# Kernel optimization log

Hardware: AMD Instinct MI355X
Metric: run time of the kernel (lower is better)

The kernel has to match this reference:

```python
import jax, jax.numpy as jnp
import numpy as np

N_NODES = 80000; N_EDGES = 480000; F_IN = 5; DIM = 3; HID = 128; LAT = 128
N_POOLS = 2; RATIO = 0.5; SLOPE = 0.2  # GATv2 leaky_relu negative slope


def _p(key, shape, fan_in):
    return jax.random.normal(key, shape, dtype=jnp.float32) / np.sqrt(float(fan_in))


def setup_inputs() -> dict:
    key = jax.random.key(0)
    ks = jax.random.split(key, 20)
    c0 = F_IN + DIM + 3          # conv0 in-channels: x | pos | y*ones
    ch = HID + DIM               # all later convs / pool gnns: h | pos
    return dict(
        x=jax.random.normal(ks[0], (N_NODES, F_IN), dtype=jnp.float32),
        y=jax.random.normal(ks[1], (1,), dtype=jnp.float32),
        pos=jax.random.normal(ks[2], (N_NODES, DIM), dtype=jnp.float32),
        edge_index=jax.random.randint(ks[3], (2, N_EDGES), 0, N_NODES),
        Wl0=_p(ks[4], (c0, HID), c0), Wr0=_p(ks[5], (c0, HID), c0),
        We0=_p(ks[6], (DIM, HID), DIM), a0=_p(ks[7], (HID,), HID), b0=jnp.zeros((HID,), jnp.float32),
        # stacked convs: [conv1, pool-conv1, pool-conv2, last-conv], all (HID+DIM)->HID(=LAT)
        Wls=_p(ks[8], (4, ch, HID), ch), Wrs=_p(ks[9], (4, ch, HID), ch),
        Wes=_p(ks[10], (4, DIM, HID), DIM), atts=_p(ks[11], (4, HID), HID), bs=jnp.zeros((4, HID), jnp.float32),
        # SAGPool score GNNs: (HID+DIM)->1
        pWl=_p(ks[12], (N_POOLS, ch, 1), ch), pWr=_p(ks[13], (N_POOLS, ch, 1), ch),
        pWe=_p(ks[14], (N_POOLS, DIM, 1), DIM), pa=_p(ks[15], (N_POOLS, 1), 1), pb=jnp.zeros((N_POOLS, 1), jnp.float32),
        linW=_p(ks[16], (LAT, LAT), LAT), linb=jnp.zeros((LAT,), jnp.float32),
    )


def _gatv2(xf, ei, ea, Wl, Wr, We, att, b):
    # PyG GATv2Conv, heads=1, add_self_loops=True, fill_value='mean' for loop edge_attr
    N = xf.shape[0]
    src = jnp.asarray(ei[0]); dst = jnp.asarray(ei[1])
    ones = jnp.ones((src.shape[0],), dtype=xf.dtype)
    deg = jax.ops.segment_sum(ones, dst, num_segments=N)
    loop_attr = jax.ops.segment_sum(ea, dst, num_segments=N) / jnp.clip(deg, 1.0)[:, None]
    ar = jnp.arange(N)
    src_f = jnp.concatenate([src, ar]); dst_f = jnp.concatenate([dst, ar])
    ea_f = jnp.concatenate([ea, loop_attr], axis=0)
    xl = xf @ Wl; xr = xf @ Wr                              # [N, C]
    m = jax.nn.leaky_relu(xl[src_f] + xr[dst_f] + ea_f @ We, SLOPE)  # [Ef, C]
    logits = m @ att                                        # [Ef]
    mx = jax.ops.segment_max(logits, dst_f, num_segments=N)
    z = jnp.exp(logits - mx[dst_f])
    denom = jax.ops.segment_sum(z, dst_f, num_segments=N)
    alpha = z / denom[dst_f]
    return jax.ops.segment_sum(alpha[:, None] * xl[src_f], dst_f, num_segments=N) + b


def _augment(ei, N):
    # adj + adj@adj (sparse coo with coalesce): union of 1-hop and 2-hop edges
    s, t = ei[0].astype(np.int64), ei[1].astype(np.int64)
    order = np.argsort(s, kind='stable')
    t2 = t[order]
    counts = np.bincount(s, minlength=N)
    starts = np.concatenate([[0], np.cumsum(counts)[:-1]])
    lens = counts[t]                      # out-degree of each edge's target (middle node)
    total = int(lens.sum())
    within = np.arange(total) - np.repeat(np.cumsum(lens) - lens, lens)
    b = t2[np.repeat(starts[t], lens) + within]
    a = np.repeat(s, lens)
    key = np.unique(np.concatenate([s * N + t, a * N + b]))
    return np.stack([key // N, key % N])


def _filter_adj(ei, perm, N):
    mask = np.zeros(N, dtype=bool); mask[perm] = True
    keep = mask[ei[0]] & mask[ei[1]]
    relabel = np.full(N, -1, dtype=np.int64); relabel[perm] = np.arange(len(perm))
    return relabel[ei[:, keep]]


def _encoder(fl, ei0, structs):
    (x, y, pos, Wl0, Wr0, We0, a0, b0, Wls, Wrs, Wes, atts, bs,
     pWl, pWr, pWe, pa, pb, linW, linb) = fl
    capture = structs is None
    recs = []
    ei = ei0
    ea = pos[ei[1]] - pos[ei[0]]
    h = jax.nn.elu(_gatv2(jnp.concatenate([x, pos, y * jnp.ones_like(pos)], 1), ei, ea, Wl0, Wr0, We0, a0, b0))
    h = jax.nn.elu(_gatv2(jnp.concatenate([h, pos], 1), ei, ea, Wls[0], Wrs[0], Wes[0], atts[0], bs[0]))
    pe = [ei]; pp = [pos]; eas = [ea]
    N = x.shape[0]
    for l in range(N_POOLS):
        ei_aug = _augment(np.asarray(ei), N) if capture else structs[l][0]
        ea_aug = pos[ei_aug[1]] - pos[ei_aug[0]]
        score = jnp.tanh(_gatv2(jnp.concatenate([h, pos], 1), ei_aug, ea_aug,
                                pWl[l], pWr[l], pWe[l], pa[l], pb[l])[:, 0])
        k = int(np.ceil(RATIO * N))
        if capture:
            _, perm = jax.lax.top_k(score, k)
            perm = np.asarray(perm)
            ei_next = _filter_adj(np.asarray(ei), perm, N)
            recs.append((ei_aug, perm, ei_next))
        else:
            _, perm, ei_next = structs[l]
        h = h[perm] * score[perm][:, None]
        pos = pos[perm]
        ei = ei_next; N = k
        ea = pos[ei[1]] - pos[ei[0]]
        pe.insert(0, ei); pp.insert(0, pos); eas.insert(0, ea)
        h = jax.nn.elu(_gatv2(jnp.concatenate([h, pos], 1), ei, ea,
                              Wls[l + 1], Wrs[l + 1], Wes[l + 1], atts[l + 1], bs[l + 1]))
    h = jax.nn.elu(_gatv2(jnp.concatenate([h, pos], 1), ei, ea, Wls[3], Wrs[3], Wes[3], atts[3], bs[3]))
    out = h @ linW + linb   # torch.vmap(self.lin)
    return out, pe, pp, eas, recs


def reference(x, y, pos, edge_index, Wl0, Wr0, We0, a0, b0, Wls, Wrs, Wes, atts, bs,
              pWl, pWr, pWe, pa, pb, linW, linb):
    fl = (x, y, pos, Wl0, Wr0, We0, a0, b0, Wls, Wrs, Wes, atts, bs,
          pWl, pWr, pWe, pa, pb, linW, linb)
    out, pe, pp, eas, _ = _encoder(fl, np.asarray(edge_index), None)
    return (out,) + tuple(jnp.asarray(e) for e in pe) + tuple(pp) + tuple(eas)
```

## Files before the change

### kernel.cpp

```cpp
#include <hip/hip_runtime.h>

typedef unsigned long long ull;

#define NN0 80000
#define EE0 480000
#define KK1 40000
#define KK2 20000
#define FLATMAX 8000000
#define SCH 4096
#define CDIV(a,b) (((a)+(b)-1)/(b))
#define HBINS (1<<21)
#define LSW 1024
#define FCAP 512

#define C_E1 2
#define C_E2 3
#define C_M0 5
#define C_M1 6

__device__ __forceinline__ int getE(const int* p, int s){ if(!p) return s; int e=*p; return e<s? e : s; }
__device__ __forceinline__ float leakyf(float x){ return x>0.f? x : 0.2f*x; }
__device__ __forceinline__ double leakyd(double x){ return x>0.0? x : 0.2*x; }
__device__ __forceinline__ float eluf(float x){ return x>0.f? x : (expf(x)-1.f); }

__device__ __forceinline__ ull encd(double f){ ull u=(ull)__double_as_longlong(f); return (u>>63)? ~u : (u|0x8000000000000000ULL); }

template<int MODE, bool DUAL>
__global__ void gemm_k(const float* __restrict__ F1, const float* __restrict__ pos,
                       const float* __restrict__ yv,
                       const float* __restrict__ W1, const float* __restrict__ W2,
                       const float* __restrict__ bias,
                       float* __restrict__ O1, float* __restrict__ O2, int N)
{
  const int K = MODE==0? 11 : (MODE==1? 131 : 128);
  __shared__ float lf[32][132];
  int t = threadIdx.x;
  int row0 = blockIdx.x*32;

  if(MODE==0){
    for(int i=t;i<32*11;i+=256){
      int r=i/11, k=i-r*11; int row=row0+r;
      float f=0.f;
      if(row<N) f = (k<5)? F1[(size_t)row*5+k] : (k<8? pos[(size_t)row*3+(k-5)] : yv[0]);
      lf[r][k]=f;
    }
  } else {
    for(int i=t;i<32*32;i+=256){
      int r=i>>5, c4=i&31; int row=row0+r;
      float4 v; v.x=0.f;v.y=0.f;v.z=0.f;v.w=0.f;
      if(row<N) v = *(const float4*)(F1+(size_t)row*128+c4*4);
      *(float4*)(&lf[r][c4*4]) = v;
    }
    if(MODE==1){
      for(int i=t;i<32*3;i+=256){
        int r=i/3, d=i-r*3; int row=row0+r;
        lf[r][128+d] = (row<N)? pos[(size_t)row*3+d] : 0.f;
      }
    }
  }
  __syncthreads();

  int cg = t&31, rg = t>>5;
  int g = cg*4;
  int rbase = rg*4;

  float acc1[4][4]; float acc2[4][4];
  #pragma unroll
  for(int rr=0;rr<4;rr++)
    #pragma unroll
    for(int c=0;c<4;c++){ acc1[rr][c]=0.f; acc2[rr][c]=0.f; }

  #pragma unroll 4
  for(int k=0;k<K;k++){
    float4 w = *(const float4*)(W1 + (size_t)k*128 + g);
    float4 v; v.x=0.f;v.y=0.f;v.z=0.f;v.w=0.f;
    if(DUAL) v = *(const float4*)(W2 + (size_t)k*128 + g);
    #pragma unroll
    for(int rr=0;rr<4;rr++){
      float f = lf[rbase+rr][k];
      acc1[rr][0]+=f*w.x; acc1[rr][1]+=f*w.y; acc1[rr][2]+=f*w.z; acc1[rr][3]+=f*w.w;
      if(DUAL){ acc2[rr][0]+=f*v.x; acc2[rr][1]+=f*v.y; acc2[rr][2]+=f*v.z; acc2[rr][3]+=f*v.w; }
    }
  }

  float4 bb; bb.x=0.f;bb.y=0.f;bb.z=0.f;bb.w=0.f;
  if(bias) bb = *(const float4*)(bias+g);
  #pragma unroll
  for(int rr=0;rr<4;rr++){
    int row = row0 + rbase + rr;
    if(row<N){
      float4 r1; r1.x=acc1[rr][0]+bb.x; r1.y=acc1[rr][1]+bb.y; r1.z=acc1[rr][2]+bb.z; r1.w=acc1[rr][3]+bb.w;
      *(float4*)(O1+(size_t)row*128+g) = r1;
      if(DUAL){
        float4 r2; r2.x=acc2[rr][0]; r2.y=acc2[rr][1]; r2.z=acc2[rr][2]; r2.w=acc2[rr][3];
        *(float4*)(O2+(size_t)row*128+g) = r2;
      }
    }
  }
}

__global__ void scan_p1(const int* __restrict__ in, const int* pN, int Ns, int* __restrict__ bsums){
  __shared__ int red[256];
  int n = getE(pN,Ns);
  int base = blockIdx.x*SCH;
  int s=0;
  for(int i=base+threadIdx.x; i<base+SCH; i+=256) if(i<n) s+=in[i];
  red[threadIdx.x]=s; __syncthreads();
  for(int o=128;o;o>>=1){ if(threadIdx.x<(unsigned)o) red[threadIdx.x]+=red[threadIdx.x+o]; __syncthreads(); }
  if(threadIdx.x==0) bsums[blockIdx.x]=red[0];
}
__global__ void scan_p2(int* bsums, int nb){
  __shared__ int lds[256];
  int t=threadIdx.x;
  int v = (t<nb)? bsums[t] : 0;
  lds[t]=v; __syncthreads();
  for(int o=1;o<256;o<<=1){ int u=0; if(t>=o) u=lds[t-o]; __syncthreads(); lds[t]+=u; __syncthreads(); }
  if(t<nb) bsums[t]=lds[t]-v;
}
__global__ void scan_p3(const int* __restrict__ in, int* __restrict__ out, const int* pN, int Ns,
                        const int* __restrict__ bsums, int* total){
  __shared__ int tsum[256];
  int n = getE(pN,Ns);
  int base = blockIdx.x*SCH + threadIdx.x*16;
  int v[16]; int s=0;
  #pragma unroll
  for(int q=0;q<16;q++){ int i=base+q; int xv=(i<n)? in[i]:0; v[q]=s; s+=xv; }
  tsum[threadIdx.x]=s; __syncthreads();
  int mine=s;
  for(int o=1;o<256;o<<=1){ int u=0; if(threadIdx.x>=(unsigned)o) u=tsum[threadIdx.x-o]; __syncthreads(); tsum[threadIdx.x]+=u; __syncthreads(); }
  int pre = bsums[blockIdx.x] + tsum[threadIdx.x] - mine;
  #pragma unroll
  for(int q=0;q<16;q++){
    int i=base+q;
    if(i<=n){
      int val = pre+v[q];
      out[i]=val;
      if(i==n && total) *total=val;
    }
  }
}

__global__ void count_src(const int* __restrict__ es, const int* pE, int Es, int* cnts){
  int e = blockIdx.x*256+threadIdx.x; int E = getE(pE,Es); if(e>=E) return;
  atomicAdd(&cnts[es[e]], 1);
}
__global__ void fill_eord(const int* __restrict__ es, const int* __restrict__ ed, const int* pE, int Es,
                          const int* __restrict__ dstarts, int* cursor, int* insrc){
  int e = blockIdx.x*256+threadIdx.x; int E = getE(pE,Es); if(e>=E) return;
  int d = ed[e];
  int p = dstarts[d] + atomicAdd(&cursor[d],1);
  insrc[p] = es[e];
}

__global__ void feat_fused(const int* __restrict__ insrc, const int* __restrict__ dstarts,
                           const float* __restrict__ A, const float* __restrict__ B,
                           const float* __restrict__ pos,
                           const float* __restrict__ We, const float* __restrict__ att,
                           const float* __restrict__ bias, float* __restrict__ h, int N)
{
  __shared__ float lgAll[4][FCAP];
  int wv = threadIdx.x>>6, lane = threadIdx.x&63;
  int w = blockIdx.x*4 + wv;
  bool active = (w<N);
  if(!active) w = N-1;
  float* lg = lgAll[wv];
  int r0=dstarts[w], r1=dstarts[w+1]; int din=r1-r0;
  int c=lane, c2=lane+64;
  float B0 = B[(size_t)w*128+c], B1 = B[(size_t)w*128+c2];
  float We0c=We[c], We1c=We[128+c], We2c=We[256+c];
  float We0d=We[c2], We1d=We[128+c2], We2d=We[256+c2];
  float attc=att[c], attd=att[c2];
  float pw0=pos[w*3], pw1=pos[w*3+1], pw2=pos[w*3+2];

  float l0=0,l1=0,l2=0;
  for(int j=0;j<din;j++){
    int s = insrc[r0+j];
    float e0=pw0-pos[s*3], e1=pw1-pos[s*3+1], e2=pw2-pos[s*3+2];
    l0+=e0; l1+=e1; l2+=e2;
    float a0=A[(size_t)s*128+c], a1=A[(size_t)s*128+c2];
    float m1 = a0 + B0 + e0*We0c + e1*We1c + e2*We2c;
    float m2 = a1 + B1 + e0*We0d + e1*We1d + e2*We2d;
    float p = leakyf(m1)*attc + leakyf(m2)*attd;
    for(int o=32;o;o>>=1) p += __shfl_down(p,o,64);
    if(lane==0 && j<FCAP) lg[j]=p;
  }
  float inv = 1.f/fmaxf((float)din, 1.f);
  float q0=l0*inv, q1=l1*inv, q2=l2*inv;
  float a0w=A[(size_t)w*128+c], a1w=A[(size_t)w*128+c2];
  float pself;
  {
    float m1 = a0w + B0 + q0*We0c + q1*We1c + q2*We2c;
    float m2 = a1w + B1 + q0*We0d + q1*We1d + q2*We2d;
    float p = leakyf(m1)*attc + leakyf(m2)*attd;
    for(int o=32;o;o>>=1) p += __shfl_down(p,o,64);
    pself = __shfl(p,0,64);
  }
  float mx = pself;
  int dc = din<FCAP? din : FCAP;
  for(int j=lane;j<dc;j+=64) mx = fmaxf(mx, lg[j]);
  for(int o=32;o;o>>=1) mx = fmaxf(mx, __shfl_down(mx,o,64));
  mx = __shfl(mx,0,64);
  for(int j=FCAP;j<din;j++){
    int s = insrc[r0+j];
    float e0=pw0-pos[s*3], e1=pw1-pos[s*3+1], e2=pw2-pos[s*3+2];
    float a0=A[(size_t)s*128+c], a1=A[(size_t)s*128+c2];
    float m1 = a0 + B0 + e0*We0c + e1*We1c + e2*We2c;
    float m2 = a1 + B1 + e0*We0d + e1*We1d + e2*We2d;
    float p = leakyf(m1)*attc + leakyf(m2)*attd;
    for(int o=32;o;o>>=1) p += __shfl_down(p,o,64);
    p = __shfl(p,0,64);
    mx = fmaxf(mx, p);
  }

  float denom=0.f, acc0=0.f, acc1=0.f;
  for(int j=0;j<din;j++){
    int s = insrc[r0+j];
    float lgj;
    if(j<FCAP) lgj = lg[j];
    else {
      float e0=pw0-pos[s*3], e1=pw1-pos[s*3+1], e2=pw2-pos[s*3+2];
      float a0=A[(size_t)s*128+c], a1=A[(size_t)s*128+c2];
      float m1 = a0 + B0 + e0*We0c + e1*We1c + e2*We2c;
      float m2 = a1 + B1 + e0*We0d + e1*We1d + e2*We2d;
      float p = leakyf(m1)*attc + leakyf(m2)*attd;
      for(int o=32;o;o>>=1) p += __shfl_down(p,o,64);
      lgj = __shfl(p,0,64);
    }
    float z = expf(lgj - mx);
    denom += z;
    acc0 += z*A[(size_t)s*128+c];
    acc1 += z*A[(size_t)s*128+c2];
  }
  {
    float z = expf(pself - mx);
    denom += z;
    acc0 += z*a0w; acc1 += z*a1w;
  }
  float iv = 1.f/denom;
  float b0v=bias[c], b1v=bias[c2];
  acc0 = eluf(acc0*iv + b0v); acc1 = eluf(acc1*iv + b1v);
  if(active){
    h[(size_t)w*128+c ] = acc0;
    h[(size_t)w*128+c2] = acc1;
  }
}

__global__ void gemm_score(const float* __restrict__ h, const float* __restrict__ pos,
                           const float* __restrict__ pWl, const float* __restrict__ pWr,
                           double* __restrict__ xls, double* __restrict__ xrs, int N)
{
  int t = threadIdx.x;
  int lane = t&31;
  int n = blockIdx.x*8 + (t>>5);
  if(n>=N) return;
  double sl=0, sr=0;
  #pragma unroll
  for(int q=0;q<4;q++){
    int k = lane + q*32;
    double f = (double)h[(size_t)n*128+k];
    sl += f*(double)pWl[k]; sr += f*(double)pWr[k];
  }
  if(lane<3){
    double f = (double)pos[n*3+lane];
    sl += f*(double)pWl[128+lane]; sr += f*(double)pWr[128+lane];
  }
  for(int o=16;o;o>>=1){ sl += __shfl_down(sl,o,32); sr += __shfl_down(sr,o,32); }
  if(lane==0){ xls[n]=sl; xrs[n]=sr; }
}

__global__ void score_fused2(const int* __restrict__ insrc, const int* __restrict__ dstarts,
                             const float* __restrict__ pos,
                             const double* __restrict__ xls, const double* __restrict__ xrs,
                             const float* __restrict__ pWe, const float* __restrict__ paP,
                             const float* __restrict__ pbP,
                             double* __restrict__ score, int N)
{
  __shared__ int lsAll[4][LSW];
  int wv = threadIdx.x>>6;
  int lane = threadIdx.x&63;
  int w = blockIdx.x*4 + wv;
  bool active = (w<N);
  if(!active) w = N-1;
  int* ls = lsAll[wv];
  int r0=dstarts[w], r1=dstarts[w+1]; int din=r1-r0;
  for(int j=lane;j<din && j<LSW;j+=64) ls[j]=insrc[r0+j];
  __syncthreads();
  int off = din<LSW? din : LSW;
  for(int base=0; base<din && base<LSW; base+=64){
    int t = base + lane;
    int u0=0, len=0;
    if(t<din && t<LSW){
      int u = ls[t];
      u0 = dstarts[u]; len = dstarts[u+1]-u0;
    }
    int pre = len;
    #pragma unroll
    for(int o=1;o<64;o<<=1){ int v=__shfl_up(pre,o,64); if(lane>=o) pre+=v; }
    int tot = __shfl(pre, 63, 64);
    int myoff = off + pre - len;
    for(int j=0;j<len;j++){ int p=myoff+j; if(p<LSW) ls[p]=insrc[u0+j]; }
    off += tot;
  }
  int d = off<LSW? off : LSW;
  __syncthreads();

  float pd0=pos[w*3], pd1=pos[w*3+1], pd2=pos[w*3+2];
  double w0=(double)pWe[0], w1=(double)pWe[1], w2=(double)pWe[2], pa=(double)paP[0];
  double xrd=xrs[w];
  ull umask=0;
  double lgv[4], xv[4];
  double mx=-1e300, s0=0,s1=0,s2=0; int ucnt=0;
  #pragma unroll
  for(int it=0; it<4; it++){
    int j = lane + it*64;
    if(j<d){
      int s = ls[j];
      bool uniq = true;
      for(int q=0;q<j;q++) if(ls[q]==s){ uniq=false; break; }
      if(uniq){
        umask |= 1ULL<<it;
        ucnt++;
        double e0=(double)(pd0-pos[s*3]), e1=(double)(pd1-pos[s*3+1]), e2=(double)(pd2-pos[s*3+2]);
        s0+=e0; s1+=e1; s2+=e2;
        double xl = xls[s];
        double lg = leakyd(xl+xrd + e0*w0+e1*w1+e2*w2) * pa;
        lgv[it]=lg; xv[it]=xl;
        mx = fmax(mx, lg);
      }
    }
  }
  int nb=4;
  for(int j=lane+256; j<d; j+=64, nb++){
    int s = ls[j];
    bool uniq = true;
    for(int q=0;q<j;q++) if(ls[q]==s){ uniq=false; break; }
    if(uniq){
      umask |= 1ULL<<nb;
      ucnt++;
      double e0=(double)(pd0-pos[s*3]), e1=(double)(pd1-pos[s*3+1]), e2=(double)(pd2-pos[s*3+2]);
      s0+=e0; s1+=e1; s2+=e2;
      double lg = leakyd(xls[s]+xrd + e0*w0+e1*w1+e2*w2) * pa;
      mx = fmax(mx, lg);
    }
  }
  for(int o=32;o;o>>=1){
    mx = fmax(mx, __shfl_down(mx,o,64));
    s0 += __shfl_down(s0,o,64);
    s1 += __shfl_down(s1,o,64);
    s2 += __shfl_down(s2,o,64);
    ucnt += __shfl_down(ucnt,o,64);
  }
  mx=__shfl(mx,0,64); s0=__shfl(s0,0,64); s1=__shfl(s1,0,64); s2=__shfl(s2,0,64); ucnt=__shfl(ucnt,0,64);
  double invd = 1.0/(double)(ucnt>0? ucnt : 1);
  double lg_self = leakyd(xls[w]+xrd + (s0*invd)*w0 + (s1*invd)*w1 + (s2*invd)*w2) * pa;
  mx = fmax(mx, lg_self);
  double den=0, acc=0;
  #pragma unroll
  for(int it=0; it<4; it++){
    if((umask>>it)&1ULL){
      double z = exp(lgv[it]-mx);
      den += z; acc += z*xv[it];
    }
  }
  nb=4;
  for(int j=lane+256; j<d; j+=64, nb++){
    if((umask>>nb)&1ULL){
      int s = ls[j];
      double e0=(double)(pd0-pos[s*3]), e1=(double)(pd1-pos[s*3+1]), e2=(double)(pd2-pos[s*3+2]);
      double lg = leakyd(xls[s]+xrd + e0*w0+e1*w1+e2*w2) * pa;
      double z = exp(lg-mx);
      den += z; acc += z*xls[s];
    }
  }
  for(int o=32;o;o>>=1){
    den += __shfl_down(den,o,64);
    acc += __shfl_down(acc,o,64);
  }
  if(lane==0 && active){
    double z = exp(lg_self-mx);
    den += z; acc += z*xls[w];
    score[w] = tanh(acc/den + (double)pbP[0]);
  }
}

__global__ void enc_scores(const double* __restrict__ score, int N, ull* __restrict__ ek,
                           int* __restrict__ rank){
  int i = blockIdx.x*256+threadIdx.x; if(i>=N) return;
  ek[i] = encd(score[i]);
  rank[i] = 0x3f3f3f3f;
}
__global__ void hist_g(const ull* __restrict__ ek, int N, int shift, const ull* __restrict__ selT,
                       int* __restrict__ hist){
  int i = blockIdx.x*256+threadIdx.x; if(i>=N) return;
  ull key = ek[i];
  if(shift+21 < 64){
    if((key >> (shift+21)) != ((*selT) >> (shift+21))) return;
  }
  atomicAdd(&hist[(int)((key>>shift)&0x1FFFFF)], 1);
}
__global__ void part21(const int* __restrict__ hist, int* __restrict__ partial){
  __shared__ int red[256];
  int b = blockIdx.x;
  int s=0;
  for(int i=threadIdx.x;i<1024;i+=256) s += hist[b*1024+i];
  red[threadIdx.x]=s; __syncthreads();
  for(int o=128;o;o>>=1){ if(threadIdx.x<(unsigned)o) red[threadIdx.x]+=red[threadIdx.x+o]; __syncthreads(); }
  if(threadIdx.x==0) partial[b]=red[0];
}
__global__ void findbin_g(const int* __restrict__ partial, const int* __restrict__ hist,
                          ull* __restrict__ selT, int* __restrict__ selRB, int k, int shift){
  __shared__ int ts[256];
  __shared__ int cstar, rbase;
  int t=threadIdx.x;
  int keff = k - *selRB;
  int s8[8]; int mysum=0;
  #pragma unroll
  for(int q=0;q<8;q++){ s8[q]=partial[t*8+q]; mysum+=s8[q]; }
  ts[t]=mysum; __syncthreads();
  for(int o=1;o<256;o<<=1){ int u=(t+o<256)? ts[t+o]:0; __syncthreads(); ts[t]+=u; __syncthreads(); }
  int after = (t<255)? ts[t+1] : 0;
  if(ts[t] >= keff && after < keff){
    int run = after;
    for(int q=7;q>=0;q--){
      if(run < keff && run + s8[q] >= keff){ cstar = t*8+q; rbase = run; }
      run += s8[q];
    }
  }
  __syncthreads();
  int cs=cstar, rb=rbase;
  int b4[4]; int ms=0;
  #pragma unroll
  for(int q=0;q<4;q++){ b4[q]=hist[cs*1024 + t*4 + q]; ms+=b4[q]; }
  ts[t]=ms; __syncthreads();
  for(int o=1;o<256;o<<=1){ int u=(t+o<256)? ts[t+o]:0; __syncthreads(); ts[t]+=u; __syncthreads(); }
  int after2 = (t<255)? ts[t+1] : 0;
  if(rb+ts[t] >= keff && rb+after2 < keff){
    int run = rb+after2;
    for(int q=3;q>=0;q--){
      if(run < keff && run + b4[q] >= keff){
        *selT |= ((ull)(cs*1024 + t*4 + q)) << shift;
        *selRB = (k - keff) + run;
      }
      run += b4[q];
    }
  }
}
__global__ void rank_hist(const ull* __restrict__ ek, int N, const ull* __restrict__ selT,
                          int* __restrict__ hist){
  int i = blockIdx.x*256+threadIdx.x; if(i>=N) return;
  ull key = ek[i]; if(key < *selT) return;
  int dg = (int)((~key >> 43) & 0x1FFFFF);
  atomicAdd(&hist[dg], 1);
}
__global__ void binscan(const int* __restrict__ hist, const int* __restrict__ p2,
                        int* __restrict__ binstarts){
  __shared__ int ts[256];
  int b = blockIdx.x, t = threadIdx.x;
  int v[4]; int s=0;
  #pragma unroll
  for(int q=0;q<4;q++){ v[q]=s; s+=hist[b*1024 + t*4 + q]; }
  ts[t]=s; __syncthreads();
  int mine=s;
  for(int o=1;o<256;o<<=1){ int u=0; if(t>=(unsigned)o) u=ts[t-o]; __syncthreads(); ts[t]+=u; __syncthreads(); }
  int pre = p2[b] + ts[t] - mine;
  #pragma unroll
  for(int q=0;q<4;q++) binstarts[b*1024 + t*4 + q] = pre + v[q];
  if(b==2047 && t==255) binstarts[HBINS] = p2[b] + ts[255];
}
__global__ void rank_fill(const ull* __restrict__ ek, int N, const ull* __restrict__ selT,
                          const int* __restrict__ binstarts, int* __restrict__ hist,
                          ull* __restrict__ mkeys, int* __restrict__ midx){
  int i = blockIdx.x*256+threadIdx.x; if(i>=N) return;
  ull key = ek[i]; if(key < *selT) return;
  int dg = (int)((~key >> 43) & 0x1FFFFF);
  int o = atomicSub(&hist[dg], 1) - 1;
  int p = binstarts[dg] + o;
  mkeys[p] = key; midx[p] = i;
}
__global__ void rank_within(const int* __restrict__ binstarts,
                            const ull* __restrict__ mkeys, const int* __restrict__ midx,
                            int* __restrict__ rank, int Nmax){
  int m = blockIdx.x*256+threadIdx.x; if(m>=Nmax) return;
  int total = binstarts[HBINS]; if(m>=total) return;
  ull key = mkeys[m]; int ii = midx[m];
  int dg = (int)((~key >> 43) & 0x1FFFFF);
  int s = binstarts[dg], e = binstarts[dg+1];
  int cnt = 0;
  for(int j=s;j<e;j++){
    ull kj = mkeys[j];
    cnt += (kj > key) || (kj == key && midx[j] < ii);
  }
  rank[ii] = s + cnt;
}
__global__ void scatter_perm(const int* __restrict__ rank, int N, int k, int* __restrict__ perm){
  int i = blockIdx.x*256+threadIdx.x; if(i>=N) return;
  int r = rank[i]; if(r<k) perm[r]=i;
}
__global__ void pool_gather(const float* __restrict__ h, const double* __restrict__ score,
                            const int* __restrict__ perm, int k, float* __restrict__ outA){
  int idx = blockIdx.x*256+threadIdx.x; if(idx>=k*32) return;
  int r = idx>>5, g = (idx&31)*4;
  int p = perm[r]; float sc = (float)score[p];
  const float4 x = *(const float4*)(h + (size_t)p*128 + g);
  float4 o; o.x=x.x*sc; o.y=x.y*sc; o.z=x.z*sc; o.w=x.w*sc;
  *(float4*)(outA + (size_t)r*128 + g) = o;
}
__global__ void pos_gather(const float* __restrict__ posc, const int* __restrict__ perm, int k, float* __restrict__ posn){
  int idx = blockIdx.x*256+threadIdx.x; if(idx>=k*3) return;
  int r = idx/3, j = idx-r*3;
  posn[idx] = posc[perm[r]*3+j];
}

__global__ void filter_flags(const int* __restrict__ es, const int* __restrict__ ed, const int* pE, int Es,
                             const int* __restrict__ rank, int k, int* __restrict__ flags){
  int e = blockIdx.x*256+threadIdx.x; int E = getE(pE,Es); if(e>=E) return;
  flags[e] = (rank[es[e]]<k && rank[ed[e]]<k) ? 1 : 0;
}
__global__ void filter_write(const int* __restrict__ es, const int* __restrict__ ed, const int* pE, int Es,
                             const int* __restrict__ rank, int k, const int* __restrict__ scanout,
                             int* __restrict__ ns, int* __restrict__ nd){
  int e = blockIdx.x*256+threadIdx.x; int E = getE(pE,Es); if(e>=E) return;
  int rs = rank[es[e]], rd = rank[ed[e]];
  if(rs<k && rd<k){ int p = scanout[e]; ns[p]=rs; nd[p]=rd; }
}

__global__ void calc_offsets(const int* __restrict__ cnt, long long* __restrict__ offs){
  if(blockIdx.x==0 && threadIdx.x==0){
    long long E1 = cnt[C_E1], E2 = cnt[C_E2];
    long long o = (long long)KK2*128;
    offs[0]=0;
    offs[1]=o; o += 2*E2;
    offs[2]=o; o += 2*E1;
    offs[3]=o; o += 2*(long long)EE0;
    offs[4]=o; o += (long long)KK2*3;
    offs[5]=o; o += (long long)KK1*3;
    offs[6]=o; o += (long long)NN0*3;
    offs[7]=o; o += 3*E2;
    offs[8]=o; o += 3*E1;
    offs[9]=o;
  }
}
__global__ void emit_pe(const int* __restrict__ s, const int* __restrict__ d, const int* pE, int Es,
                        const long long* __restrict__ offs, int oi, float* __restrict__ out){
  int e = blockIdx.x*256+threadIdx.x; int E = getE(pE,Es); if(e>=E) return;
  long long o = offs[oi];
  out[o+e]   = (float)s[e];
  out[o+E+e] = (float)d[e];
}
__global__ void emit_pp(const float* __restrict__ p, int n, const long long* __restrict__ offs, int oi, float* __restrict__ out){
  int i = blockIdx.x*256+threadIdx.x; if(i>=n) return;
  out[offs[oi]+i] = p[i];
}
__global__ void emit_eas(const int* __restrict__ s, const int* __restrict__ d, const int* pE, int Es,
                         const float* __restrict__ pos, const long long* __restrict__ offs, int oi, float* __restrict__ out){
  int e = blockIdx.x*256+threadIdx.x; int E = getE(pE,Es); if(e>=E) return;
  long long o = offs[oi];
  int ss=s[e], dd=d[e];
  out[o+3*e+0] = pos[dd*3+0]-pos[ss*3+0];
  out[o+3*e+1] = pos[dd*3+1]-pos[ss*3+1];
  out[o+3*e+2] = pos[dd*3+2]-pos[ss*3+2];
}

extern "C" void kernel_launch(void* const* d_in, const int* in_sizes, int n_in,
                              void* d_out, int out_size, void* d_ws, size_t ws_size,
                              hipStream_t stream)
{
  const float* x    = (const float*)d_in[0];
  const float* yv   = (const float*)d_in[1];
  const float* pos0 = (const float*)d_in[2];
  const int*   ei   = (const int*)d_in[3];
  const float* Wl0  = (const float*)d_in[4];
  const float* Wr0  = (const float*)d_in[5];
  const float* We0  = (const float*)d_in[6];
  const float* a0   = (const float*)d_in[7];
  const float* b0   = (const float*)d_in[8];
  const float* Wls  = (const float*)d_in[9];
  const float* Wrs  = (const float*)d_in[10];
  const float* Wes  = (const float*)d_in[11];
  const float* atts = (const float*)d_in[12];
  const float* bs   = (const float*)d_in[13];
  const float* pWl  = (const float*)d_in[14];
  const float* pWr  = (const float*)d_in[15];
  const float* pWe  = (const float*)d_in[16];
  const float* pa   = (const float*)d_in[17];
  const float* pb   = (const float*)d_in[18];
  const float* linW = (const float*)d_in[19];
  const float* linb = (const float*)d_in[20];
  float* out = (float*)d_out;

  const int* eisrc = ei;
  const int* eidst = ei + EE0;

  char* base = (char*)d_ws; size_t off = 0;
  auto alloc = [&](size_t b)->void*{
    off = (off + 255) & ~(size_t)255;
    void* p = base + off; off += b; return p;
  };
  int*       cnt     = (int*)alloc(64*4);
  long long* offs    = (long long*)alloc(16*8);
  int*       bsums   = (int*)alloc(256*4);
  ull*       sel     = (ull*)alloc(2*8);
  int*       hist    = (int*)alloc((size_t)HBINS*4);
  int*       partial = (int*)alloc(2048*4);
  int*       partial2= (int*)alloc(2304*4);
  double*    xls     = (double*)alloc((size_t)NN0*8);
  double*    xrs     = (double*)alloc((size_t)NN0*8);
  double*    score   = (double*)alloc((size_t)NN0*8);
  ull*       ek      = (ull*)alloc((size_t)NN0*8);
  int*       rank    = (int*)alloc((size_t)NN0*4);
  int*       perm    = (int*)alloc((size_t)NN0*4);
  int*       cursor  = (int*)alloc((size_t)NN0*4);
  int*       ccnt    = (int*)alloc((size_t)NN0*4);
  int*       dstarts = (int*)alloc((size_t)(NN0+1)*4);
  int*       insrc   = (int*)alloc((size_t)EE0*4);
  int*       flags   = (int*)alloc((size_t)EE0*4);
  int*       scanout = (int*)alloc((size_t)(EE0+1)*4);
  int*       eb0s    = (int*)alloc((size_t)EE0*4);
  int*       eb0d    = (int*)alloc((size_t)EE0*4);
  int*       eb1s    = (int*)alloc((size_t)EE0*4);
  int*       eb1d    = (int*)alloc((size_t)EE0*4);
  float*     pos1    = (float*)alloc((size_t)KK1*12);
  float*     pos2    = (float*)alloc((size_t)KK2*12);
  float*     A       = (float*)alloc((size_t)NN0*128*4);
  float*     B       = (float*)alloc((size_t)NN0*128*4);
  float*     h       = (float*)alloc((size_t)NN0*128*4);
  void*      uni     = alloc((size_t)(EE0+FLATMAX)*8);
  if(off > ws_size) return;

  int*    binstarts= (int*)uni;
  ull*    mkeys    = (ull*)((int*)uni + (HBINS + 256));
  int*    midx     = (int*)(mkeys + NN0);
  ull*    selT  = sel;
  int*    selRB = (int*)(sel+1);

  hipMemsetAsync(cnt, 0, 64*4, stream);

  auto scan = [&](const int* in, int* sout, const int* pN, int Ns, int* total){
    int nb = CDIV(Ns+1, SCH);
    scan_p1<<<nb,256,0,stream>>>(in,pN,Ns,bsums);
    scan_p2<<<1,256,0,stream>>>(bsums,nb);
    scan_p3<<<nb,256,0,stream>>>(in,sout,pN,Ns,bsums,total);
  };

  auto build_csr_dst = [&](const int* es, const int* ed, const int* pE, int Emax, int N){
    hipMemsetAsync(ccnt,0,(size_t)N*4,stream);
    count_src<<<CDIV(Emax,256),256,0,stream>>>(ed,pE,Emax,ccnt);
    scan(ccnt,dstarts,nullptr,N,nullptr);
    hipMemsetAsync(cursor,0,(size_t)N*4,stream);
    fill_eord<<<CDIV(Emax,256),256,0,stream>>>(es,ed,pE,Emax,dstarts,cursor,insrc);
  };

  auto feat_conv = [&](const float* Wl, const float* Wr, const float* We, const float* att, const float* bias,
                       int N, const float* pcur, bool conv0mode){
    if(conv0mode)
      gemm_k<0,true><<<CDIV(N,32),256,0,stream>>>(x,pcur,yv,Wl,Wr,nullptr,A,B,N);
    else
      gemm_k<1,true><<<CDIV(N,32),256,0,stream>>>(h,pcur,nullptr,Wl,Wr,nullptr,A,B,N);
    feat_fused<<<CDIV(N,4),256,0,stream>>>(insrc,dstarts,A,B,pcur,We,att,bias,h,N);
  };

  auto pool = [&](int l, int N, int k, const int* es, const int* ed, const int* pE, int Emax,
                  const float* pcur, float* pnext, int* ns, int* nd, int eslot){
    gemm_score<<<CDIV(N,8),256,0,stream>>>(h,pcur,pWl+l*131,pWr+l*131,xls,xrs,N);
    score_fused2<<<CDIV(N,4),256,0,stream>>>(insrc,dstarts,pcur,xls,xrs,pWe+l*3,pa+l,pb+l,score,N);
    enc_scores<<<CDIV(N,256),256,0,stream>>>(score,N,ek,rank);
    hipMemsetAsync(sel,0,16,stream);
    for(int r=0;r<2;r++){
      int sh = 43 - 21*r;
      hipMemsetAsync(hist,0,(size_t)HBINS*4,stream);
      hist_g<<<CDIV(N,256),256,0,stream>>>(ek,N,sh,selT,hist);
      part21<<<2048,256,0,stream>>>(hist,partial);
      findbin_g<<<1,256,0,stream>>>(partial,hist,selT,selRB,k,sh);
    }
    hipMemsetAsync(hist,0,(size_t)HBINS*4,stream);
    rank_hist  <<<CDIV(N,256),256,0,stream>>>(ek,N,selT,hist);
    part21     <<<2048,256,0,stream>>>(hist,partial);
    scan(partial,partial2,nullptr,2048,nullptr);
    binscan    <<<2048,256,0,stream>>>(hist,partial2,binstarts);
    rank_fill  <<<CDIV(N,256),256,0,stream>>>(ek,N,selT,binstarts,hist,mkeys,midx);
    rank_within<<<CDIV(N,256),256,0,stream>>>(binstarts,mkeys,midx,rank,N);
    scatter_perm<<<CDIV(N,256),256,0,stream>>>(rank,N,k,perm);
    pool_gather<<<CDIV(k*32,256),256,0,stream>>>(h,score,perm,k,A);
    hipMemcpyAsync(h,A,(size_t)k*128*4,hipMemcpyDeviceToDevice,stream);
    pos_gather<<<CDIV(k*3,256),256,0,stream>>>(pcur,perm,k,pnext);
    filter_flags<<<CDIV(Emax,256),256,0,stream>>>(es,ed,pE,Emax,rank,k,flags);
    scan(flags,scanout,pE,Emax,cnt+eslot);
    filter_write<<<CDIV(Emax,256),256,0,stream>>>(es,ed,pE,Emax,rank,k,scanout,ns,nd);
  };

  build_csr_dst(eisrc,eidst,nullptr,EE0, NN0);
  feat_conv(Wl0,Wr0,We0,a0,b0, NN0, pos0, true);
  feat_conv(Wls+0*16768,Wrs+0*16768,Wes+0*384,atts+0*128,bs+0*128, NN0, pos0, false);
  pool(0, NN0, KK1, eisrc,eidst,nullptr,EE0, pos0,pos1, eb0s,eb0d, C_E1);
  build_csr_dst(eb0s,eb0d,cnt+C_E1,EE0, KK1);
  feat_conv(Wls+1*16768,Wrs+1*16768,Wes+1*384,atts+1*128,bs+1*128, KK1, pos1, false);
  pool(1, KK1, KK2, eb0s,eb0d,cnt+C_E1,EE0, pos1,pos2, eb1s,eb1d, C_E2);
  build_csr_dst(eb1s,eb1d,cnt+C_E2,EE0, KK2);
  feat_conv(Wls+2*16768,Wrs+2*16768,Wes+2*384,atts+2*128,bs+2*128, KK2, pos2, false);
  feat_conv(Wls+3*16768,Wrs+3*16768,Wes+3*384,atts+3*128,bs+3*128, KK2, pos2, false);
  gemm_k<2,false><<<CDIV(KK2,32),256,0,stream>>>(h,nullptr,nullptr,linW,nullptr,linb,out,nullptr,KK2);

  calc_offsets<<<1,32,0,stream>>>(cnt,offs);
  emit_pe <<<CDIV(EE0,256),256,0,stream>>>(eb1s,eb1d,cnt+C_E2,EE0,offs,1,out);
  emit_pe <<<CDIV(EE0,256),256,0,stream>>>(eb0s,eb0d,cnt+C_E1,EE0,offs,2,out);
  emit_pe <<<CDIV(EE0,256),256,0,stream>>>(eisrc,eidst,nullptr,EE0,offs,3,out);
  emit_pp <<<CDIV(KK2*3,256),256,0,stream>>>(pos2,KK2*3,offs,4,out);
  emit_pp <<<CDIV(KK1*3,256),256,0,stream>>>(pos1,KK1*3,offs,5,out);
  emit_pp <<<CDIV(NN0*3,256),256,0,stream>>>(pos0,NN0*3,offs,6,out);
  emit_eas<<<CDIV(EE0,256),256,0,stream>>>(eb1s,eb1d,cnt+C_E2,EE0,pos2,offs,7,out);
  emit_eas<<<CDIV(EE0,256),256,0,stream>>>(eb0s,eb0d,cnt+C_E1,EE0,pos1,offs,8,out);
  emit_eas<<<CDIV(EE0,256),256,0,stream>>>(eisrc,eidst,nullptr,EE0,pos0,offs,9,out);
}
```

Measured before the change: 1.805 ms.

## Fuse edge-filter with scan, fold score encoding, batch output emit kernels

Replaces the flag/scan/write edge-filter pipeline with a two-pass fused scan that recomputes the rank predicate and writes compacted edges directly, removing the flags and scanout buffers. Score encoding moves into the score kernel, and rank initialisation becomes a memset. The first histogram clear is hoisted out of the pool loop. The nine output emit launches are merged into three launches using a y-grid dimension. This cuts kernel launches and global traffic in exchange for recomputing the rank lookups in two passes, and it relies on the histogram being zero again when the second pool starts.

```diff
diff --git a/kernel.cpp b/kernel.cpp
--- a/kernel.cpp
+++ b/kernel.cpp
@@ -137,6 +137,50 @@
       out[i]=val;
       if(i==n && total) *total=val;
     }
+  }
+}
+
+__global__ void fscan_p1(const int* __restrict__ es, const int* __restrict__ ed, const int* pE, int Es,
+                         const int* __restrict__ rank, int k, int* __restrict__ bsums){
+  __shared__ int red[256];
+  int n = getE(pE,Es);
+  int base = blockIdx.x*SCH;
+  int s=0;
+  for(int i=base+threadIdx.x; i<base+SCH; i+=256)
+    if(i<n) s += (rank[es[i]]<k && rank[ed[i]]<k) ? 1 : 0;
+  red[threadIdx.x]=s; __syncthreads();
+  for(int o=128;o;o>>=1){ if(threadIdx.x<(unsigned)o) red[threadIdx.x]+=red[threadIdx.x+o]; __syncthreads(); }
+  if(threadIdx.x==0) bsums[blockIdx.x]=red[0];
+}
+__global__ void fscan_p3(const int* __restrict__ es, const int* __restrict__ ed, const int* pE, int Es,
+                         const int* __restrict__ rank, int k, const int* __restrict__ bsums,
+                         int* __restrict__ ns, int* __restrict__ nd, int* total){
+  __shared__ int tsum[256];
+  int n = getE(pE,Es);
+  int base = blockIdx.x*SCH + threadIdx.x*16;
+  int v[16]; int rs[16], rd[16]; unsigned fm=0; int s=0;
+  #pragma unroll
+  for(int q=0;q<16;q++){
+    int i=base+q; int xv=0;
+    if(i<n){
+      int a=rank[es[i]], b=rank[ed[i]];
+      rs[q]=a; rd[q]=b;
+      if(a<k && b<k){ xv=1; fm |= 1u<<q; }
+    }
+    v[q]=s; s+=xv;
+  }
+  tsum[threadIdx.x]=s; __syncthreads();
+  int mine=s;
+  for(int o=1;o<256;o<<=1){ int u=0; if(threadIdx.x>=(unsigned)o) u=tsum[threadIdx.x-o]; __syncthreads(); tsum[threadIdx.x]+=u; __syncthreads(); }
+  int pre = bsums[blockIdx.x] + tsum[threadIdx.x] - mine;
+  #pragma unroll
+  for(int q=0;q<16;q++){
+    int i=base+q;
+    if(i<n && ((fm>>q)&1u)){
+      int p = pre+v[q];
+      ns[p]=rs[q]; nd[p]=rd[q];
+    }
+    if(i==n && total) *total = pre+v[q];
   }
 }
 
@@ -273,7 +317,7 @@
                              const double* __restrict__ xls, const double* __restrict__ xrs,
                              const float* __restrict__ pWe, const float* __restrict__ paP,
                              const float* __restrict__ pbP,
-                             double* __restrict__ score, int N)
+                             double* __restrict__ score, ull* __restrict__ ek, int N)
 {
   __shared__ int lsAll[4][LSW];
   int wv = threadIdx.x>>6;
@@ -379,16 +423,12 @@
   if(lane==0 && active){
     double z = exp(lg_self-mx);
     den += z; acc += z*xls[w];
-    score[w] = tanh(acc/den + (double)pbP[0]);
-  }
-}
-
-__global__ void enc_scores(const double* __restrict__ score, int N, ull* __restrict__ ek,
-                           int* __restrict__ rank){
-  int i = blockIdx.x*256+threadIdx.x; if(i>=N) return;
-  ek[i] = encd(score[i]);
-  rank[i] = 0x3f3f3f3f;
-}
+    double sc = tanh(acc/den + (double)pbP[0]);
+    score[w] = sc;
+    ek[w] = encd(sc);
+  }
+}
+
 __global__ void hist_g(const ull* __restrict__ ek, int N, int shift, const ull* __restrict__ selT,
                        int* __restrict__ hist){
   int i = blockIdx.x*256+threadIdx.x; if(i>=N) return;
@@ -509,19 +549,6 @@
   int idx = blockIdx.x*256+threadIdx.x; if(idx>=k*3) return;
   int r = idx/3, j = idx-r*3;
   posn[idx] = posc[perm[r]*3+j];
-}
-
-__global__ void filter_flags(const int* __restrict__ es, const int* __restrict__ ed, const int* pE, int Es,
-                             const int* __restrict__ rank, int k, int* __restrict__ flags){
-  int e = blockIdx.x*256+threadIdx.x; int E = getE(pE,Es); if(e>=E) return;
-  flags[e] = (rank[es[e]]<k && rank[ed[e]]<k) ? 1 : 0;
-}
-__global__ void filter_write(const int* __restrict__ es, const int* __restrict__ ed, const int* pE, int Es,
-                             const int* __restrict__ rank, int k, const int* __restrict__ scanout,
-                             int* __restrict__ ns, int* __restrict__ nd){
-  int e = blockIdx.x*256+threadIdx.x; int E = getE(pE,Es); if(e>=E) return;
-  int rs = rank[es[e]], rd = rank[ed[e]];
-  if(rs<k && rd<k){ int p = scanout[e]; ns[p]=rs; nd[p]=rd; }
 }
 
 __global__ void calc_offsets(const int* __restrict__ cnt, long long* __restrict__ offs){
@@ -540,20 +567,44 @@
     offs[9]=o;
   }
 }
-__global__ void emit_pe(const int* __restrict__ s, const int* __restrict__ d, const int* pE, int Es,
-                        const long long* __restrict__ offs, int oi, float* __restrict__ out){
-  int e = blockIdx.x*256+threadIdx.x; int E = getE(pE,Es); if(e>=E) return;
+__global__ void emit3_pe(const int* __restrict__ s2, const int* __restrict__ d2, const int* pE2,
+                         const int* __restrict__ s1, const int* __restrict__ d1, const int* pE1,
+                         const int* __restrict__ s0, const int* __restrict__ d0,
+                         const long long* __restrict__ offs, float* __restrict__ out){
+  int e = blockIdx.x*256+threadIdx.x;
+  int L = blockIdx.y;
+  const int* s; const int* d; int E; int oi;
+  if(L==0){ s=s2; d=d2; E=getE(pE2,EE0); oi=1; }
+  else if(L==1){ s=s1; d=d1; E=getE(pE1,EE0); oi=2; }
+  else { s=s0; d=d0; E=EE0; oi=3; }
+  if(e>=E) return;
   long long o = offs[oi];
   out[o+e]   = (float)s[e];
   out[o+E+e] = (float)d[e];
 }
-__global__ void emit_pp(const float* __restrict__ p, int n, const long long* __restrict__ offs, int oi, float* __restrict__ out){
-  int i = blockIdx.x*256+threadIdx.x; if(i>=n) return;
+__global__ void emit3_pp(const float* __restrict__ p2, const float* __restrict__ p1,
+                         const float* __restrict__ p0,
+                         const long long* __restrict__ offs, float* __restrict__ out){
+  int i = blockIdx.x*256+threadIdx.x;
+  int L = blockIdx.y;
+  const float* p; int n; int oi;
+  if(L==0){ p=p2; n=KK2*3; oi=4; }
+  else if(L==1){ p=p1; n=KK1*3; oi=5; }
+  else { p=p0; n=NN0*3; oi=6; }
+  if(i>=n) return;
   out[offs[oi]+i] = p[i];
 }
-__global__ void emit_eas(const int* __restrict__ s, const int* __restrict__ d, const int* pE, int Es,
-                         const float* __restrict__ pos, const long long* __restrict__ offs, int oi, float* __restrict__ out){
-  int e = blockIdx.x*256+threadIdx.x; int E = getE(pE,Es); if(e>=E) return;
+__global__ void emit3_eas(const int* __restrict__ s2, const int* __restrict__ d2, const int* pE2, const float* __restrict__ q2,
+                          const int* __restrict__ s1, const int* __restrict__ d1, const int* pE1, const float* __restrict__ q1,
+                          const int* __restrict__ s0, const int* __restrict__ d0, const float* __restrict__ q0,
+                          const long long* __restrict__ offs, float* __restrict__ out){
+  int e = blockIdx.x*256+threadIdx.x;
+  int L = blockIdx.y;
+  const int* s; const int* d; const float* pos; int E; int oi;
+  if(L==0){ s=s2; d=d2; pos=q2; E=getE(pE2,EE0); oi=7; }
+  else if(L==1){ s=s1; d=d1; pos=q1; E=getE(pE1,EE0); oi=8; }
+  else { s=s0; d=d0; pos=q0; E=EE0; oi=9; }
+  if(e>=E) return;
   long long o = offs[oi];
   int ss=s[e], dd=d[e];
   out[o+3*e+0] = pos[dd*3+0]-pos[ss*3+0];
@@ -613,8 +664,6 @@
   int*       ccnt    = (int*)alloc((size_t)NN0*4);
   int*       dstarts = (int*)alloc((size_t)(NN0+1)*4);
   int*       insrc   = (int*)alloc((size_t)EE0*4);
-  int*       flags   = (int*)alloc((size_t)EE0*4);
-  int*       scanout = (int*)alloc((size_t)(EE0+1)*4);
   int*       eb0s    = (int*)alloc((size_t)EE0*4);
   int*       eb0d    = (int*)alloc((size_t)EE0*4);
   int*       eb1s    = (int*)alloc((size_t)EE0*4);
@@ -634,6 +683,7 @@
   int*    selRB = (int*)(sel+1);
 
   hipMemsetAsync(cnt, 0, 64*4, stream);
+  hipMemsetAsync(hist, 0, (size_t)HBINS*4, stream);
 
   auto scan = [&](const int* in, int* sout, const int* pN, int Ns, int* total){
     int nb = CDIV(Ns+1, SCH);
@@ -661,13 +711,13 @@
 
   auto pool = [&](int l, int N, int k, const int* es, const int* ed, const int* pE, int Emax,
                   const float* pcur, float* pnext, int* ns, int* nd, int eslot){
+    hipMemsetAsync(rank, 0x3f, (size_t)N*4, stream);
     gemm_score<<<CDIV(N,8),256,0,stream>>>(h,pcur,pWl+l*131,pWr+l*131,xls,xrs,N);
-    score_fused2<<<CDIV(N,4),256,0,stream>>>(insrc,dstarts,pcur,xls,xrs,pWe+l*3,pa+l,pb+l,score,N);
-    enc_scores<<<CDIV(N,256),256,0,stream>>>(score,N,ek,rank);
+    score_fused2<<<CDIV(N,4),256,0,stream>>>(insrc,dstarts,pcur,xls,xrs,pWe+l*3,pa+l,pb+l,score,ek,N);
     hipMemsetAsync(sel,0,16,stream);
     for(int r=0;r<2;r++){
       int sh = 43 - 21*r;
-      hipMemsetAsync(hist,0,(size_t)HBINS*4,stream);
+      if(r>0) hipMemsetAsync(hist,0,(size_t)HBINS*4,stream);
       hist_g<<<CDIV(N,256),256,0,stream>>>(ek,N,sh,selT,hist);
       part21<<<2048,256,0,stream>>>(hist,partial);
       findbin_g<<<1,256,0,stream>>>(partial,hist,selT,selRB,k,sh);
@@ -683,9 +733,12 @@
     pool_gather<<<CDIV(k*32,256),256,0,stream>>>(h,score,perm,k,A);
     hipMemcpyAsync(h,A,(size_t)k*128*4,hipMemcpyDeviceToDevice,stream);
     pos_gather<<<CDIV(k*3,256),256,0,stream>>>(pcur,perm,k,pnext);
-    filter_flags<<<CDIV(Emax,256),256,0,stream>>>(es,ed,pE,Emax,rank,k,flags);
-    scan(flags,scanout,pE,Emax,cnt+eslot);
-    filter_write<<<CDIV(Emax,256),256,0,stream>>>(es,ed,pE,Emax,rank,k,scanout,ns,nd);
+    {
+      int nb = CDIV(Emax+1, SCH);
+      fscan_p1<<<nb,256,0,stream>>>(es,ed,pE,Emax,rank,k,bsums);
+      scan_p2<<<1,256,0,stream>>>(bsums,nb);
+      fscan_p3<<<nb,256,0,stream>>>(es,ed,pE,Emax,rank,k,bsums,ns,nd,cnt+eslot);
+    }
   };
 
   build_csr_dst(eisrc,eidst,nullptr,EE0, NN0);
@@ -701,13 +754,13 @@
   gemm_k<2,false><<<CDIV(KK2,32),256,0,stream>>>(h,nullptr,nullptr,linW,nullptr,linb,out,nullptr,KK2);
 
   calc_offsets<<<1,32,0,stream>>>(cnt,offs);
-  emit_pe <<<CDIV(EE0,256),256,0,stream>>>(eb1s,eb1d,cnt+C_E2,EE0,offs,1,out);
-  emit_pe <<<CDIV(EE0,256),256,0,stream>>>(eb0s,eb0d,cnt+C_E1,EE0,offs,2,out);
-  emit_pe <<<CDIV(EE0,256),256,0,stream>>>(eisrc,eidst,nullptr,EE0,offs,3,out);
-  emit_pp <<<CDIV(KK2*3,256),256,0,stream>>>(pos2,KK2*3,offs,4,out);
-  emit_pp <<<CDIV(KK1*3,256),256,0,stream>>>(pos1,KK1*3,offs,5,out);
-  emit_pp <<<CDIV(NN0*3,256),256,0,stream>>>(pos0,NN0*3,offs,6,out);
-  emit_eas<<<CDIV(EE0,256),256,0,stream>>>(eb1s,eb1d,cnt+C_E2,EE0,pos2,offs,7,out);
-  emit_eas<<<CDIV(EE0,256),256,0,stream>>>(eb0s,eb0d,cnt+C_E1,EE0,pos1,offs,8,out);
-  emit_eas<<<CDIV(EE0,256),256,0,stream>>>(eisrc,eidst,nullptr,EE0,pos0,offs,9,out);
-}
+  {
+    dim3 g(CDIV(EE0,256),3);
+    emit3_pe <<<g,256,0,stream>>>(eb1s,eb1d,cnt+C_E2, eb0s,eb0d,cnt+C_E1, eisrc,eidst, offs,out);
+    emit3_eas<<<g,256,0,stream>>>(eb1s,eb1d,cnt+C_E2,pos2, eb0s,eb0d,cnt+C_E1,pos1, eisrc,eidst,pos0, offs,out);
+  }
+  {
+    dim3 g(CDIV(NN0*3,256),3);
+    emit3_pp <<<g,256,0,stream>>>(pos2,pos1,pos0,offs,out);
+  }
+}
```

New measurement: 1.802 ms. No clear change (-0.2%).
